# Performance work log

Measured on AMD Instinct MI355X. Metric: run time of the kernel, lower is better.

Reference implementation:

```python
import jax, jax.numpy as jnp
import numpy as np

N_NODE = 20000
EPS = 1e-6


def setup_inputs() -> dict:
    N, E, B, D, NEG, L, R2 = N_NODE, 250000, 8, 32, 32, 6, 100
    ks = jax.random.split(jax.random.key(0), 12)
    return {
        "edge_src": jax.random.randint(ks[0], (E,), 0, N),
        "edge_dst": jax.random.randint(ks[1], (E,), 0, N),
        "edge_type": jax.random.randint(ks[2], (E,), 0, R2),
        "h_index": jax.random.randint(ks[3], (B,), 0, N),
        "t_index": jax.random.randint(ks[4], (B, NEG), 0, N),
        "r_index": jax.random.randint(ks[5], (B,), 0, R2),
        "query_emb": jax.random.normal(ks[6], (R2, D), jnp.float32) * 0.1,
        "Wr": jax.random.normal(ks[7], (L, R2 * D, D), jnp.float32) * (1.0 / np.sqrt(D)),
        "br": jnp.zeros((L, R2 * D), jnp.float32),
        "Wl": jax.random.normal(ks[8], (L, D, 13 * D), jnp.float32) * (1.0 / np.sqrt(13 * D)),
        "bl": jnp.zeros((L, D), jnp.float32),
        "W1": jax.random.normal(ks[9], (2 * D, 2 * D), jnp.float32) * (1.0 / np.sqrt(2 * D)),
        "b1": jnp.zeros((2 * D,), jnp.float32),
        "W2": jax.random.normal(ks[10], (1, 2 * D), jnp.float32) * (1.0 / np.sqrt(2 * D)),
        "b2": jnp.zeros((1,), jnp.float32),
    }


def reference(edge_src, edge_dst, edge_type, h_index, t_index, r_index,
              query_emb, Wr, br, Wl, bl, W1, b1, W2, b2):
    N = N_NODE
    B = h_index.shape[0]
    D = query_emb.shape[1]
    L = Wr.shape[0]

    query = query_emb[r_index]                                   # (B, D)
    # boundary condition: scatter query embedding onto head nodes
    boundary = jnp.zeros((N, B, D), query.dtype).at[h_index, jnp.arange(B)].add(query)

    # aggregation segments: real edges + one self-loop (boundary message) per node
    seg = jnp.concatenate([edge_dst, jnp.arange(N)])
    deg = jnp.zeros((N,), query.dtype).at[edge_dst].add(1.0) + 1.0  # degree_out + 1
    scale = jnp.log(deg)
    scale = scale / scale.mean()
    # PNA degree scalers: identity, amplification, attenuation
    scales = jnp.stack([jnp.ones_like(scale), scale, 1.0 / jnp.clip(scale, 1e-2)], -1)  # (N, 3)

    x = boundary                                                 # (N, B, D)
    for i in range(L):
        # query-dependent relation embeddings
        rel = (query @ Wr[i].T + br[i]).reshape(B, -1, D)        # (B, 2R, D)
        edge_rel = rel[:, edge_type].transpose(1, 0, 2)          # (E, B, D)
        msg = x[edge_src] * edge_rel                             # distmult message
        msg = jnp.concatenate([msg, boundary], axis=0)           # (E+N, B, D)
        s1 = jax.ops.segment_sum(msg, seg, num_segments=N)
        s2 = jax.ops.segment_sum(msg * msg, seg, num_segments=N)
        mean = s1 / deg[:, None, None]
        sq_mean = s2 / deg[:, None, None]
        mx = jax.ops.segment_max(msg, seg, num_segments=N)
        mn = jax.ops.segment_min(msg, seg, num_segments=N)
        std = jnp.sqrt(jnp.clip(sq_mean - mean * mean, EPS))
        feat = jnp.stack([mean, mx, mn, std], -1).reshape(N, B, 4 * D)
        update = (feat[..., None] * scales[:, None, None, :]).reshape(N, B, 12 * D)
        x = jax.nn.relu(jnp.concatenate([x, update], -1) @ Wl[i].T + bl[i])

    out = jnp.concatenate([x, jnp.broadcast_to(query[None], (N, B, D))], -1)  # (N, B, 2D)
    feat_t = out[t_index, jnp.arange(B)[:, None]]                # (B, NEG, 2D)
    h = jax.nn.relu(feat_t @ W1.T + b1)
    score = (h @ W2.T + b2)[..., 0]                              # (B, NEG)
    return score
```

## Files before the change

kernel.cpp:

```cpp
#include <hip/hip_runtime.h>
#include <math.h>

namespace {

constexpr int N   = 20000;
constexpr int E   = 250000;
constexpr int B   = 8;
constexpr int D   = 32;
constexpr int R2  = 100;
constexpr int L   = 6;
constexpr int NEG = 32;
constexpr float EPSF = 1e-6f;

constexpr int BD = B * D;
constexpr int NPB = 8;
constexpr int WSZ  = 26624;
constexpr int NSCB = (N + 255) / 256;
constexpr int NBLK = N / NPB;
constexpr int SBLK = 64 * 128;
constexpr int GPB  = 10;
constexpr int GBLK = NBLK / GPB;
constexpr int RELSZ = L * B * R2 * D;

typedef __attribute__((ext_vector_type(8))) short bf16x8;
typedef __attribute__((ext_vector_type(4))) float f32x4;
typedef _Float16 half4_t __attribute__((ext_vector_type(4)));
typedef _Float16 half8_t __attribute__((ext_vector_type(8)));
typedef float float4_t __attribute__((ext_vector_type(4)));

__device__ inline unsigned short f2bf(float x) {
  unsigned int u = __float_as_uint(x);
  unsigned int r = u + 0x7FFF + ((u >> 16) & 1);
  return (unsigned short)(r >> 16);
}
__device__ inline float bf2f(unsigned short h) {
  return __uint_as_float(((unsigned int)h) << 16);
}
__device__ inline void split2(float v, unsigned short& hi, unsigned short& lo) {
  hi = f2bf(v);
  lo = f2bf(v - bf2f(hi));
}

__global__ void k_init(unsigned int* x0i, int* cnt, float* meanacc) {
  int i = blockIdx.x * blockDim.x + threadIdx.x;
  int stride = gridDim.x * blockDim.x;
  for (int t = i; t < N * BD / 2; t += stride) x0i[t] = 0u;
  for (int t = i; t < N; t += stride) cnt[t] = 0;
  if (i == 0) meanacc[0] = 0.f;
}

__global__ void k_countq(const int* __restrict__ edge_dst, int* cnt,
                         const int* __restrict__ r_index, const int* __restrict__ h_index,
                         const float* __restrict__ query_emb, float* query, _Float16* x0) {
  if (blockIdx.x == gridDim.x - 1) {
    int tid = threadIdx.x;
    int b = tid >> 5, d = tid & 31;
    float q = query_emb[r_index[b] * D + d];
    query[tid] = q;
    x0[h_index[b] * BD + tid] = (_Float16)q;
    return;
  }
  int e = blockIdx.x * blockDim.x + threadIdx.x;
  if (e < E) atomicAdd(&cnt[edge_dst[e]], 1);
}

__global__ void k_scanA(const int* __restrict__ cnt, int* row_start, int* bsum,
                        int* fill, float* meanacc) {
  __shared__ int wsum[4];
  __shared__ float fsum[4];
  int tid = threadIdx.x;
  int lane = tid & 63, wv = tid >> 6;
  int i = blockIdx.x * 256 + tid;
  int v = (i < N) ? cnt[i] : 0;
  int x = v;
  for (int o = 1; o < 64; o <<= 1) {
    int y = __shfl_up(x, o, 64);
    if (lane >= o) x += y;
  }
  if (lane == 63) wsum[wv] = x;
  __syncthreads();
  int add = 0;
  for (int w = 0; w < wv; ++w) add += wsum[w];
  if (i < N) {
    row_start[i] = x - v + add;
    fill[i] = 0;
  }
  if (tid == 255) bsum[blockIdx.x] = add + x;
  float lv = (i < N) ? logf((float)(v + 1)) : 0.f;
  for (int o = 32; o > 0; o >>= 1) lv += __shfl_down(lv, o, 64);
  if (lane == 0) fsum[wv] = lv;
  __syncthreads();
  if (tid == 0) atomicAdd(meanacc, fsum[0] + fsum[1] + fsum[2] + fsum[3]);
}

__global__ void k_scanB(const int* __restrict__ bsum, int* boff, int* row_start) {
  int lane = threadIdx.x;
  int a0 = (lane < NSCB) ? bsum[lane] : 0;
  int a1 = (64 + lane < NSCB) ? bsum[64 + lane] : 0;
  int x = a0;
  for (int o = 1; o < 64; o <<= 1) {
    int y = __shfl_up(x, o, 64);
    if (lane >= o) x += y;
  }
  int tot0 = __shfl(x, 63, 64);
  int x1 = a1;
  for (int o = 1; o < 64; o <<= 1) {
    int y = __shfl_up(x1, o, 64);
    if (lane >= o) x1 += y;
  }
  if (lane < NSCB) boff[lane] = x - a0;
  if (64 + lane < NSCB) boff[64 + lane] = tot0 + x1 - a1;
  if (lane == 63) row_start[N] = tot0 + __shfl(x1, 63, 64);
}

__global__ void k_scanC(int* row_start, const int* __restrict__ boff) {
  int i = blockIdx.x * 256 + threadIdx.x;
  if (i < N) row_start[i] += boff[blockIdx.x];
}

__global__ void k_scatter(const int* __restrict__ edge_src, const int* __restrict__ edge_dst,
                          const int* __restrict__ edge_type, const int* __restrict__ row_start,
                          int* fill, int* packed) {
  int e = blockIdx.x * blockDim.x + threadIdx.x;
  if (e < E) {
    int dn = edge_dst[e];
    int pos = atomicAdd(&fill[dn], 1);
    packed[row_start[dn] + pos] = edge_src[e] | (edge_type[e] << 16);
  }
}

__global__ void k_scales(const int* __restrict__ cnt, const float* __restrict__ meanacc,
                         float* scales) {
  int i = blockIdx.x * blockDim.x + threadIdx.x;
  if (i < N) {
    float m = meanacc[0] / (float)N;
    float s = logf((float)(cnt[i] + 1)) / m;
    scales[i * 3 + 0] = 1.f;
    scales[i * 3 + 1] = s;
    scales[i * 3 + 2] = 1.f / fmaxf(s, 0.01f);
  }
}

__global__ void k_prep(const float* __restrict__ query, const float* __restrict__ Wr,
                       const float* __restrict__ br, _Float16* rel,
                       const float* __restrict__ Wl, short* WT) {
  int o = blockIdx.x * blockDim.x + threadIdx.x;
  if (o < RELSZ) {
    int d = o & 31;
    int r = (o >> 5) % R2;
    int b = (o / (R2 * D)) % B;
    int l = o / (B * R2 * D);
    int rd = r * D + d;
    const float4* wrow = (const float4*)(Wr + ((size_t)l * R2 * D + rd) * D);
    const float* q = query + b * D;
    float acc = br[l * R2 * D + rd];
#pragma unroll
    for (int k = 0; k < 8; ++k) {
      float4 w4 = wrow[k];
      acc = fmaf(q[4 * k + 0], w4.x, acc);
      acc = fmaf(q[4 * k + 1], w4.y, acc);
      acc = fmaf(q[4 * k + 2], w4.z, acc);
      acc = fmaf(q[4 * k + 3], w4.w, acc);
    }
    rel[o] = (_Float16)acc;
    return;
  }
  int t0 = o - RELSZ;
  if (t0 >= L * 13312) return;
  int l = t0 / 13312, t = t0 % 13312;
  int j = t / 416, k = t % 416;
  float v = Wl[(size_t)l * 13312 + j * 416 + k];
  unsigned short hi, lo;
  split2(v, hi, lo);
  short* wt = WT + (size_t)l * WSZ;
  if (k < 32) {
    int dx = j * 32 + k;
    wt[dx] = (short)hi;
    wt[1024 + dx] = (short)lo;
  } else {
    int u = k - 32;
    int f = u / 3, s = u % 3;
    int df = (s * 32 + j) * 128 + f;
    wt[2048 + df] = (short)hi;
    wt[14336 + df] = (short)lo;
  }
}

__global__ __launch_bounds__(128) void k_agg(
    const _Float16* __restrict__ xin, const _Float16* __restrict__ rel_l,
    short* __restrict__ stath,
    const int* __restrict__ row_start, const int* __restrict__ packed,
    const int* __restrict__ h_index, const float* __restrict__ query) {
  int tid = threadIdx.x;
  int lane = tid & 63;
  int wv = __builtin_amdgcn_readfirstlane(tid >> 6);
  int node = blockIdx.x * 2 + wv;

  int ch4 = 4 * lane;
  int b = lane >> 3;
  int d0 = ch4 & 31;
  int hb = h_index[b];
  const _Float16* relb4 = rel_l + b * (R2 * D) + d0;
  const _Float16* xch = xin + ch4;
  int rs = row_start[node];
  int cntE = row_start[node + 1] - rs;

  float4_t s1 = {0.f, 0.f, 0.f, 0.f}, s2 = {0.f, 0.f, 0.f, 0.f};
  half4_t mxh = {(_Float16)-INFINITY, (_Float16)-INFINITY, (_Float16)-INFINITY, (_Float16)-INFINITY};
  half4_t mnh = {(_Float16)INFINITY, (_Float16)INFINITY, (_Float16)INFINITY, (_Float16)INFINITY};

  auto accp = [&](half4_t xv, half4_t rv) {
    half4_t m = xv * rv;
    mxh = __builtin_elementwise_max(mxh, m);
    mnh = __builtin_elementwise_min(mnh, m);
    float4_t mf = __builtin_convertvector(m, float4_t);
#pragma unroll
    for (int c = 0; c < 4; ++c) {
      s1[c] += mf[c];
      s2[c] = fmaf(mf[c], mf[c], s2[c]);
    }
  };

  int nfull = cntE >> 3;
  for (int t = 0; t < nfull; ++t) {
    int j0 = t * 8;
    int pk[8];
#pragma unroll
    for (int u = 0; u < 8; ++u) pk[u] = packed[rs + j0 + u];
    half4_t xv[8], rv[8];
#pragma unroll
    for (int u = 0; u < 8; ++u) xv[u] = *(const half4_t*)&xch[(pk[u] & 0xFFFF) * BD];
#pragma unroll
    for (int u = 0; u < 8; ++u) rv[u] = *(const half4_t*)&relb4[(pk[u] >> 16) * D];
#pragma unroll
    for (int u = 0; u < 8; ++u) accp(xv[u], rv[u]);
  }
  int rem = cntE & 7;
  if (rem) {
    int j0 = nfull * 8;
    int last = cntE - 1;
    int pk[8];
#pragma unroll
    for (int u = 0; u < 8; ++u) {
      int jj = j0 + u;
      pk[u] = packed[rs + (jj < cntE ? jj : last)];
    }
    half4_t xv[8], rv[8];
#pragma unroll
    for (int u = 0; u < 8; ++u) xv[u] = *(const half4_t*)&xch[(pk[u] & 0xFFFF) * BD];
#pragma unroll
    for (int u = 0; u < 8; ++u) rv[u] = *(const half4_t*)&relb4[(pk[u] >> 16) * D];
#pragma unroll
    for (int u = 0; u < 7; ++u)
      if (u < rem) accp(xv[u], rv[u]);
  }
  float4_t mxF = __builtin_convertvector(mxh, float4_t);
  float4_t mnF = __builtin_convertvector(mnh, float4_t);
  {
    const float* q4 = &query[ch4];
    bool isb = (hb == node);
#pragma unroll
    for (int c = 0; c < 4; ++c) {
      float m = isb ? q4[c] : 0.f;
      s1[c] += m;
      s2[c] = fmaf(m, m, s2[c]);
      mxF[c] = fmaxf(mxF[c], m);
      mnF[c] = fminf(mnF[c], m);
    }
  }
  float invdeg = 1.f / (float)(cntE + 1);

  unsigned int hw[8];
#pragma unroll
  for (int c = 0; c < 4; ++c) {
    float mean = s1[c] * invdeg, sq = s2[c] * invdeg;
    float sd = sqrtf(fmaxf(sq - mean * mean, EPSF));
    unsigned short h0 = f2bf(mean), h1 = f2bf(mxF[c]);
    unsigned short h2 = f2bf(mnF[c]), h3 = f2bf(sd);
    hw[2 * c]     = (unsigned)h0 | ((unsigned)h1 << 16);
    hw[2 * c + 1] = (unsigned)h2 | ((unsigned)h3 << 16);
  }
  int grp = node >> 3;
  int r = (node & 7) * 8 + b;
  short* dh = stath + (size_t)grp * SBLK + r * 128 + 4 * d0;
  *(uint4*)dh = make_uint4(hw[0], hw[1], hw[2], hw[3]);
  *(uint4*)(dh + 8) = make_uint4(hw[4], hw[5], hw[6], hw[7]);
}

struct AFrag {
  bf16x8 AH[4];
  half8_t xv;
};

__global__ __launch_bounds__(512, 2) void k_gemm(
    const _Float16* __restrict__ xin, _Float16* __restrict__ xout,
    const short* __restrict__ stath,
    const short* __restrict__ WT_l, const float* __restrict__ bl_l,
    const float* __restrict__ scales) {
  int tid = threadIdx.x;
  int lane = tid & 63;
  int wv = __builtin_amdgcn_readfirstlane(tid >> 6);
  int mt = wv >> 1, nt = wv & 1;
  int li = lane & 15, kg = lane >> 4;
  int rowA = mt * 16 + li;
  int jc = nt * 16 + li;

  const short* wxh = WT_l;
  const short* wxl = WT_l + 1024;
  const short* wfh = WT_l + 2048;

  bf16x8 BXH = *(const bf16x8*)&wxh[jc * 32 + kg * 8];
  bf16x8 BXL = *(const bf16x8*)&wxl[jc * 32 + kg * 8];
  bf16x8 BH[4][3];
#pragma unroll
  for (int step = 0; step < 4; ++step)
#pragma unroll
    for (int s = 0; s < 3; ++s)
      BH[step][s] = *(const bf16x8*)&wfh[s * 4096 + jc * 128 + step * 32 + kg * 8];

  int grp0 = blockIdx.x * GPB;

  auto loadA = [&](int g) {
    AFrag a;
    int grp = grp0 + g;
    const short* sh = stath + (size_t)grp * SBLK + rowA * 128 + kg * 8;
#pragma unroll
    for (int step = 0; step < 4; ++step) a.AH[step] = *(const bf16x8*)&sh[step * 32];
    a.xv = *(const half8_t*)&xin[(grp * NPB) * 256 + rowA * 32 + kg * 8];
    return a;
  };

  AFrag cur = loadA(0);
#pragma unroll
  for (int g = 0; g < GPB; ++g) {
    AFrag nxt;
    if (g + 1 < GPB) nxt = loadA(g + 1);

    int node0 = (grp0 + g) * NPB;
    bf16x8 axh, axl;
#pragma unroll
    for (int i = 0; i < 8; ++i) {
      unsigned short h, lo;
      split2((float)cur.xv[i], h, lo);
      axh[i] = (short)h;
      axl[i] = (short)lo;
    }

    f32x4 acc0 = {0.f, 0.f, 0.f, 0.f};
    f32x4 acc1 = {0.f, 0.f, 0.f, 0.f};
    f32x4 acc2 = {0.f, 0.f, 0.f, 0.f};

    acc0 = __builtin_amdgcn_mfma_f32_16x16x32_bf16(axl, BXH, acc0, 0, 0, 0);
    acc0 = __builtin_amdgcn_mfma_f32_16x16x32_bf16(axh, BXL, acc0, 0, 0, 0);
    acc0 = __builtin_amdgcn_mfma_f32_16x16x32_bf16(axh, BXH, acc0, 0, 0, 0);
#pragma unroll
    for (int step = 0; step < 4; ++step) {
      acc0 = __builtin_amdgcn_mfma_f32_16x16x32_bf16(cur.AH[step], BH[step][0], acc0, 0, 0, 0);
      acc1 = __builtin_amdgcn_mfma_f32_16x16x32_bf16(cur.AH[step], BH[step][1], acc1, 0, 0, 0);
      acc2 = __builtin_amdgcn_mfma_f32_16x16x32_bf16(cur.AH[step], BH[step][2], acc2, 0, 0, 0);
    }

    int rbase = mt * 16 + kg * 4;
    int node = node0 + (rbase >> 3);
    float sc1 = scales[node * 3 + 1];
    float sc2 = scales[node * 3 + 2];
    float bias = bl_l[jc & 31];
#pragma unroll
    for (int reg = 0; reg < 4; ++reg) {
      float v = acc0[reg] + sc1 * acc1[reg] + sc2 * acc2[reg] + bias;
      xout[node0 * 256 + (rbase + reg) * 32 + jc] = (_Float16)fmaxf(v, 0.f);
    }
    cur = nxt;
  }
}

__global__ void k_score(const _Float16* __restrict__ xL, const float* __restrict__ query,
                        const int* __restrict__ t_index, const float* __restrict__ W1,
                        const float* __restrict__ b1, const float* __restrict__ W2,
                        const float* __restrict__ b2, float* outp) {
  int bn = blockIdx.x;
  int b = bn >> 5;
  int j = threadIdx.x;
  __shared__ float f[64];
  int t = t_index[bn];
  f[j] = (j < 32) ? (float)xL[t * BD + b * D + j] : query[b * D + (j - 32)];
  __syncthreads();
  const float* w1r = W1 + j * 64;
  float h = b1[j];
#pragma unroll
  for (int k = 0; k < 64; ++k) h = fmaf(f[k], w1r[k], h);
  h = fmaxf(h, 0.f);
  float p = h * W2[j];
#pragma unroll
  for (int o = 32; o > 0; o >>= 1) p += __shfl_down(p, o, 64);
  if (j == 0) outp[bn] = p + b2[0];
}

}

extern "C" void kernel_launch(void* const* d_in, const int* in_sizes, int n_in,
                              void* d_out, int out_size, void* d_ws, size_t ws_size,
                              hipStream_t stream) {
  const int* edge_src   = (const int*)d_in[0];
  const int* edge_dst   = (const int*)d_in[1];
  const int* edge_type  = (const int*)d_in[2];
  const int* h_index    = (const int*)d_in[3];
  const int* t_index    = (const int*)d_in[4];
  const int* r_index    = (const int*)d_in[5];
  const float* query_emb= (const float*)d_in[6];
  const float* Wr       = (const float*)d_in[7];
  const float* br       = (const float*)d_in[8];
  const float* Wl       = (const float*)d_in[9];
  const float* bl       = (const float*)d_in[10];
  const float* W1       = (const float*)d_in[11];
  const float* b1       = (const float*)d_in[12];
  const float* W2       = (const float*)d_in[13];
  const float* b2       = (const float*)d_in[14];
  float* outp = (float*)d_out;
  (void)in_sizes; (void)n_in; (void)out_size; (void)ws_size;

  char* w = (char*)d_ws;
  auto alloc = [&](size_t bytes) {
    char* p = w;
    w += (bytes + 511) & ~(size_t)511;
    return p;
  };
  _Float16* x0   = (_Float16*)alloc(sizeof(_Float16) * N * BD);
  _Float16* x1   = (_Float16*)alloc(sizeof(_Float16) * N * BD);
  short* stath   = (short*)alloc(sizeof(short) * (size_t)NBLK * SBLK);
  _Float16* rel  = (_Float16*)alloc(sizeof(_Float16) * RELSZ);
  short* WT      = (short*)alloc(sizeof(short) * L * WSZ);
  float* query   = (float*)alloc(sizeof(float) * BD);
  float* scales  = (float*)alloc(sizeof(float) * N * 3);
  float* meanacc = (float*)alloc(sizeof(float) * 16);
  int* row_start = (int*)alloc(sizeof(int) * (N + 1));
  int* cnt       = (int*)alloc(sizeof(int) * N);
  int* fill      = (int*)alloc(sizeof(int) * N);
  int* packed    = (int*)alloc(sizeof(int) * E);
  int* bsum      = (int*)alloc(sizeof(int) * 128);
  int* boff      = (int*)alloc(sizeof(int) * 128);

  k_init<<<2048, 256, 0, stream>>>((unsigned int*)x0, cnt, meanacc);
  k_countq<<<(E + 255) / 256 + 1, 256, 0, stream>>>(edge_dst, cnt, r_index, h_index,
                                                    query_emb, query, x0);
  k_scanA<<<NSCB, 256, 0, stream>>>(cnt, row_start, bsum, fill, meanacc);
  k_scanB<<<1, 64, 0, stream>>>(bsum, boff, row_start);
  k_scanC<<<NSCB, 256, 0, stream>>>(row_start, boff);
  k_scatter<<<(E + 255) / 256, 256, 0, stream>>>(edge_src, edge_dst, edge_type,
                                                 row_start, fill, packed);
  k_scales<<<(N + 255) / 256, 256, 0, stream>>>(cnt, meanacc, scales);
  k_prep<<<(RELSZ + L * 13312 + 255) / 256, 256, 0, stream>>>(query, Wr, br, rel, Wl, WT);

  const _Float16* xin = x0;
  _Float16* xout = x1;
  for (int l = 0; l < L; ++l) {
    k_agg<<<N / 2, 128, 0, stream>>>(xin, rel + (size_t)l * B * R2 * D,
                                     stath, row_start, packed, h_index, query);
    k_gemm<<<GBLK, 512, 0, stream>>>(xin, xout, stath,
                                     WT + (size_t)l * WSZ, bl + l * D, scales);
    const _Float16* t = xout;
    xout = (_Float16*)xin;
    xin = t;
  }
  k_score<<<B * NEG, 64, 0, stream>>>(xin, query, t_index, W1, b1, W2, b2, outp);
}
```

Before: 318.9 us.

## Remap aggregation to 16 nodes per wave per batch with fp16 accumulators

The aggregation kernel is reorganised so each 64-lane wave handles one batch index for 16 nodes, with 4 lanes per node each loading 8 contiguous half channels. The wave loops up to the maximum degree among its 16 nodes and masks out edges past each node's own count. Sums and sums of squares now accumulate in packed fp16 instead of fp32. The aim is wider 16-byte gathers and more independent work per wave, at the cost of lanes idling on degree imbalance within the group and reduced accumulation precision, including overflow or cancellation risk in the variance.

```diff
diff --git a/kernel.cpp b/kernel.cpp
--- a/kernel.cpp
+++ b/kernel.cpp
@@ -24,9 +24,8 @@
 
 typedef __attribute__((ext_vector_type(8))) short bf16x8;
 typedef __attribute__((ext_vector_type(4))) float f32x4;
-typedef _Float16 half4_t __attribute__((ext_vector_type(4)));
 typedef _Float16 half8_t __attribute__((ext_vector_type(8)));
-typedef float float4_t __attribute__((ext_vector_type(4)));
+typedef _Float16 half8v __attribute__((ext_vector_type(8)));
 
 __device__ inline unsigned short f2bf(float x) {
   unsigned int u = __float_as_uint(x);
@@ -39,6 +38,12 @@
 __device__ inline void split2(float v, unsigned short& hi, unsigned short& lo) {
   hi = f2bf(v);
   lo = f2bf(v - bf2f(hi));
+}
+__device__ inline half8_t hbroad8(float v) {
+  half8_t r;
+#pragma unroll
+  for (int i = 0; i < 8; ++i) r[i] = (_Float16)v;
+  return r;
 }
 
 __global__ void k_init(unsigned int* x0i, int* cnt, float* meanacc) {
@@ -186,110 +191,90 @@
   }
 }
 
-__global__ __launch_bounds__(128) void k_agg(
+__global__ __launch_bounds__(64) void k_agg(
     const _Float16* __restrict__ xin, const _Float16* __restrict__ rel_l,
     short* __restrict__ stath,
     const int* __restrict__ row_start, const int* __restrict__ packed,
     const int* __restrict__ h_index, const float* __restrict__ query) {
-  int tid = threadIdx.x;
-  int lane = tid & 63;
-  int wv = __builtin_amdgcn_readfirstlane(tid >> 6);
-  int node = blockIdx.x * 2 + wv;
-
-  int ch4 = 4 * lane;
-  int b = lane >> 3;
-  int d0 = ch4 & 31;
-  int hb = h_index[b];
-  const _Float16* relb4 = rel_l + b * (R2 * D) + d0;
-  const _Float16* xch = xin + ch4;
+  int lane = threadIdx.x;
+  int bid = blockIdx.x;
+  int b = bid & 7;
+  int g16 = bid >> 3;
+  int e = lane >> 2;
+  int c = lane & 3;
+  int node = g16 * 16 + e;
+
   int rs = row_start[node];
   int cntE = row_start[node + 1] - rs;
-
-  float4_t s1 = {0.f, 0.f, 0.f, 0.f}, s2 = {0.f, 0.f, 0.f, 0.f};
-  half4_t mxh = {(_Float16)-INFINITY, (_Float16)-INFINITY, (_Float16)-INFINITY, (_Float16)-INFINITY};
-  half4_t mnh = {(_Float16)INFINITY, (_Float16)INFINITY, (_Float16)INFINITY, (_Float16)INFINITY};
-
-  auto accp = [&](half4_t xv, half4_t rv) {
-    half4_t m = xv * rv;
-    mxh = __builtin_elementwise_max(mxh, m);
-    mnh = __builtin_elementwise_min(mnh, m);
-    float4_t mf = __builtin_convertvector(m, float4_t);
-#pragma unroll
-    for (int c = 0; c < 4; ++c) {
-      s1[c] += mf[c];
-      s2[c] = fmaf(mf[c], mf[c], s2[c]);
-    }
-  };
-
-  int nfull = cntE >> 3;
-  for (int t = 0; t < nfull; ++t) {
-    int j0 = t * 8;
-    int pk[8];
-#pragma unroll
-    for (int u = 0; u < 8; ++u) pk[u] = packed[rs + j0 + u];
-    half4_t xv[8], rv[8];
-#pragma unroll
-    for (int u = 0; u < 8; ++u) xv[u] = *(const half4_t*)&xch[(pk[u] & 0xFFFF) * BD];
-#pragma unroll
-    for (int u = 0; u < 8; ++u) rv[u] = *(const half4_t*)&relb4[(pk[u] >> 16) * D];
-#pragma unroll
-    for (int u = 0; u < 8; ++u) accp(xv[u], rv[u]);
-  }
-  int rem = cntE & 7;
-  if (rem) {
-    int j0 = nfull * 8;
-    int last = cntE - 1;
-    int pk[8];
-#pragma unroll
-    for (int u = 0; u < 8; ++u) {
-      int jj = j0 + u;
-      pk[u] = packed[rs + (jj < cntE ? jj : last)];
-    }
-    half4_t xv[8], rv[8];
-#pragma unroll
-    for (int u = 0; u < 8; ++u) xv[u] = *(const half4_t*)&xch[(pk[u] & 0xFFFF) * BD];
-#pragma unroll
-    for (int u = 0; u < 8; ++u) rv[u] = *(const half4_t*)&relb4[(pk[u] >> 16) * D];
-#pragma unroll
-    for (int u = 0; u < 7; ++u)
-      if (u < rem) accp(xv[u], rv[u]);
-  }
-  float4_t mxF = __builtin_convertvector(mxh, float4_t);
-  float4_t mnF = __builtin_convertvector(mnh, float4_t);
-  {
-    const float* q4 = &query[ch4];
-    bool isb = (hb == node);
-#pragma unroll
-    for (int c = 0; c < 4; ++c) {
-      float m = isb ? q4[c] : 0.f;
-      s1[c] += m;
-      s2[c] = fmaf(m, m, s2[c]);
-      mxF[c] = fmaxf(mxF[c], m);
-      mnF[c] = fminf(mnF[c], m);
-    }
-  }
+  int cmax = cntE;
+#pragma unroll
+  for (int o = 4; o < 64; o <<= 1) {
+    int y = __shfl_xor(cmax, o, 64);
+    cmax = cmax > y ? cmax : y;
+  }
+  cmax = __builtin_amdgcn_readfirstlane(cmax);
+
+  const _Float16* xb   = xin + b * 32 + 8 * c;
+  const _Float16* relb = rel_l + b * (R2 * D) + 8 * c;
+  int lastc = cntE > 0 ? cntE - 1 : 0;
+
+  half8_t s1 = hbroad8(0.f), s2 = hbroad8(0.f);
+  half8_t mx = hbroad8(-INFINITY), mn = hbroad8(INFINITY);
+  half8_t z8 = hbroad8(0.f), ni8 = hbroad8(-INFINITY), pi8 = hbroad8(INFINITY);
+
+  for (int t = 0; t < cmax; t += 4) {
+    int pk[4];
+#pragma unroll
+    for (int u = 0; u < 4; ++u) {
+      int j = t + u;
+      int idx = j < cntE ? j : lastc;
+      pk[u] = packed[rs + idx];
+    }
+    half8_t xv[4], rv[4];
+#pragma unroll
+    for (int u = 0; u < 4; ++u) xv[u] = *(const half8_t*)&xb[(pk[u] & 0xFFFF) * BD];
+#pragma unroll
+    for (int u = 0; u < 4; ++u) rv[u] = *(const half8_t*)&relb[(pk[u] >> 16) * D];
+#pragma unroll
+    for (int u = 0; u < 4; ++u) {
+      bool ok = (t + u) < cntE;
+      half8_t m = xv[u] * rv[u];
+      half8_t mz = ok ? m : z8;
+      s1 += mz;
+      s2 += mz * mz;
+      mx = __builtin_elementwise_max(mx, ok ? m : ni8);
+      mn = __builtin_elementwise_min(mn, ok ? m : pi8);
+    }
+  }
+
+  bool isb = (h_index[b] == node);
   float invdeg = 1.f / (float)(cntE + 1);
-
-  unsigned int hw[8];
-#pragma unroll
-  for (int c = 0; c < 4; ++c) {
-    float mean = s1[c] * invdeg, sq = s2[c] * invdeg;
+  const float* q8 = query + b * 32 + 8 * c;
+  unsigned int hw[16];
+#pragma unroll
+  for (int cc = 0; cc < 8; ++cc) {
+    float m = isb ? q8[cc] : 0.f;
+    float S1 = (float)s1[cc] + m;
+    float S2 = fmaf(m, m, (float)s2[cc]);
+    float MX = fmaxf((float)mx[cc], m);
+    float MN = fminf((float)mn[cc], m);
+    float mean = S1 * invdeg, sq = S2 * invdeg;
     float sd = sqrtf(fmaxf(sq - mean * mean, EPSF));
-    unsigned short h0 = f2bf(mean), h1 = f2bf(mxF[c]);
-    unsigned short h2 = f2bf(mnF[c]), h3 = f2bf(sd);
-    hw[2 * c]     = (unsigned)h0 | ((unsigned)h1 << 16);
-    hw[2 * c + 1] = (unsigned)h2 | ((unsigned)h3 << 16);
+    hw[2 * cc]     = (unsigned)f2bf(mean) | ((unsigned)f2bf(MX) << 16);
+    hw[2 * cc + 1] = (unsigned)f2bf(MN)   | ((unsigned)f2bf(sd) << 16);
   }
   int grp = node >> 3;
   int r = (node & 7) * 8 + b;
-  short* dh = stath + (size_t)grp * SBLK + r * 128 + 4 * d0;
-  *(uint4*)dh = make_uint4(hw[0], hw[1], hw[2], hw[3]);
-  *(uint4*)(dh + 8) = make_uint4(hw[4], hw[5], hw[6], hw[7]);
+  short* dh = stath + (size_t)grp * SBLK + r * 128 + 32 * c;
+  *(uint4*)(dh)      = make_uint4(hw[0], hw[1], hw[2], hw[3]);
+  *(uint4*)(dh + 8)  = make_uint4(hw[4], hw[5], hw[6], hw[7]);
+  *(uint4*)(dh + 16) = make_uint4(hw[8], hw[9], hw[10], hw[11]);
+  *(uint4*)(dh + 24) = make_uint4(hw[12], hw[13], hw[14], hw[15]);
 }
 
 struct AFrag {
   bf16x8 AH[4];
-  half8_t xv;
+  half8v xv;
 };
 
 __global__ __launch_bounds__(512, 2) void k_gemm(
@@ -326,7 +311,7 @@
     const short* sh = stath + (size_t)grp * SBLK + rowA * 128 + kg * 8;
 #pragma unroll
     for (int step = 0; step < 4; ++step) a.AH[step] = *(const bf16x8*)&sh[step * 32];
-    a.xv = *(const half8_t*)&xin[(grp * NPB) * 256 + rowA * 32 + kg * 8];
+    a.xv = *(const half8v*)&xin[(grp * NPB) * 256 + rowA * 32 + kg * 8];
     return a;
   };
 
@@ -454,8 +439,8 @@
   const _Float16* xin = x0;
   _Float16* xout = x1;
   for (int l = 0; l < L; ++l) {
-    k_agg<<<N / 2, 128, 0, stream>>>(xin, rel + (size_t)l * B * R2 * D,
-                                     stath, row_start, packed, h_index, query);
+    k_agg<<<(N / 16) * 8, 64, 0, stream>>>(xin, rel + (size_t)l * B * R2 * D,
+                                           stath, row_start, packed, h_index, query);
     k_gemm<<<GBLK, 512, 0, stream>>>(xin, xout, stath,
                                      WT + (size_t)l * WSZ, bl + l * D, scales);
     const _Float16* t = xout;
```

New measurement: 372.9 us. 16.9% more time.
